# Kernel tuning notes

Measured on AMD Instinct MI355X. Metric: run time of the kernel, lower is better.

Reference implementation:

```python
import jax, jax.numpy as jnp
import numpy as np

GX, GY = 480, 360          # BEV grid (grid_size[0], grid_size[1])
C_OUT = 32                 # fea_compre
MAX_PT = 256               # max_pt_per_encode
NUM_VOX = GX * GY
BN_EPS = 1e-5


def setup_inputs() -> dict:
    key = jax.random.key(0)
    ks = jax.random.split(key, 12)
    B, N, F = 2, 100000, 7
    pt_fea = jax.random.normal(ks[0], (B, N, F), jnp.float32)
    xy_ind = jnp.stack([
        jax.random.randint(ks[1], (B, N), 0, GX),
        jax.random.randint(ks[2], (B, N), 0, GY),
    ], axis=-1).astype(jnp.int32)

    def lin(k, i, o):
        return 0.02 * jax.random.normal(k, (o, i), jnp.float32)

    inp = {"pt_fea": pt_fea, "xy_ind": xy_ind}
    dims = [(F, 64), (64, 128), (128, 256), (256, 512)]
    for j, (i, o) in enumerate(dims):
        inp[f"w{j}"] = lin(ks[3 + j], i, o)
        inp[f"b{j}"] = jnp.zeros((o,), jnp.float32)
    # BatchNorm (eval mode): bn0 on raw features, bn1..bn3 after linears 0..2
    for j, d in enumerate([F, 64, 128, 256]):
        inp[f"g{j}"] = jnp.ones((d,), jnp.float32)
        inp[f"be{j}"] = jnp.zeros((d,), jnp.float32)
        inp[f"m{j}"] = jnp.zeros((d,), jnp.float32)
        inp[f"v{j}"] = jnp.ones((d,), jnp.float32)
    inp["wc"] = lin(ks[7], 512, C_OUT)
    inp["bc"] = jnp.zeros((C_OUT,), jnp.float32)
    return inp


def _bn(x, g, b, m, v):
    return (x - m) * (g * jax.lax.rsqrt(v + BN_EPS)) + b


def reference(pt_fea, xy_ind,
              w0, b0, w1, b1, w2, b2, w3, b3,
              g0, be0, m0, v0, g1, be1, m1, v1,
              g2, be2, m2, v2, g3, be3, m3, v3,
              wc, bc):
    def pointnet(x):  # [N, 7] -> [N, 512]
        x = _bn(x, g0, be0, m0, v0)
        x = jax.nn.relu(_bn(x @ w0.T + b0, g1, be1, m1, v1))
        x = jax.nn.relu(_bn(x @ w1.T + b1, g2, be2, m2, v2))
        x = jax.nn.relu(_bn(x @ w2.T + b2, g3, be3, m3, v3))
        return x @ w3.T + b3

    def one_cloud(fea, xy):  # fea [N,7], xy [N,2] int
        N = fea.shape[0]
        vox = xy[:, 0] * GY + xy[:, 1]                      # linear voxel id
        # rank of each point within its voxel group (== grp_range_torch output)
        order = jnp.argsort(vox, stable=True)
        sid = vox[order]
        new_grp = jnp.concatenate([jnp.array([True]), sid[1:] != sid[:-1]])
        start = jax.lax.cummax(jnp.where(new_grp, jnp.arange(N), 0))
        rank_sorted = jnp.arange(N) - start
        rank = jnp.zeros((N,), rank_sorted.dtype).at[order].set(rank_sorted)
        remain = rank < MAX_PT                              # cap points per voxel

        pn = pointnet(fea)                                  # [N, 512]
        seg = jnp.where(remain, vox, NUM_VOX)               # dropped pts -> dummy seg
        maxf = jax.ops.segment_max(pn, seg, num_segments=NUM_VOX + 1)[:NUM_VOX]
        cnt = jax.ops.segment_sum(jnp.ones((N,), jnp.int32), seg,
                                  num_segments=NUM_VOX + 1)[:NUM_VOX]
        occ = (cnt > 0)[:, None]
        maxf = jnp.where(occ, maxf, 0.0)                    # kill -inf of empty voxels
        comp = jnp.where(occ, jax.nn.relu(maxf @ wc.T + bc), 0.0)  # [NUM_VOX, 32]
        return comp.reshape(GX, GY, C_OUT)

    grid = jax.vmap(one_cloud)(pt_fea, xy_ind)              # [B, GX, GY, 32]
    return jnp.transpose(grid, (0, 3, 1, 2))                # [B, 32, GX, GY]
```

## Files before the change

### kernel.cpp

```cpp
#include <hip/hip_runtime.h>

#define DEV __device__ __forceinline__

typedef _Float16 f16;
typedef __attribute__((ext_vector_type(8))) _Float16 half8;
typedef __attribute__((ext_vector_type(4))) _Float16 half4;
typedef __attribute__((ext_vector_type(4))) float floatx4;

constexpr int GXc = 480, GYc = 360;
constexpr int NVOX = GXc * GYc;
constexpr int BATCH = 2;
constexpr int NPT = 100000;
constexpr int FIN = 7;
constexpr int COUT = 32;
constexpr int MAXPT = 256;
constexpr float EPS = 1e-5f;
constexpr int NBLK = (NVOX + 255) / 256;
constexpr int FSTRIDE = NPT + 2;
constexpr int NB_PTS = (BATCH * NPT + 255) / 256;
constexpr int NB_FL  = (NPT + 255) / 256;
constexpr int ZB = 128;

DEV unsigned f2ord(float f) {
  unsigned b = __float_as_uint(f);
  return (b & 0x80000000u) ? ~b : (b | 0x80000000u);
}
DEV float ord2f(unsigned u) {
  return __uint_as_float((u & 0x80000000u) ? (u & 0x7FFFFFFFu) : ~u);
}

__global__ __launch_bounds__(256)
void k_foldcount(const float* __restrict__ w0, const float* __restrict__ b0,
                 const float* __restrict__ w1, const float* __restrict__ b1,
                 const float* __restrict__ w2, const float* __restrict__ b2,
                 const float* __restrict__ w3, const float* __restrict__ wc,
                 const float* __restrict__ g0, const float* __restrict__ be0, const float* __restrict__ m0, const float* __restrict__ v0,
                 const float* __restrict__ g1, const float* __restrict__ be1, const float* __restrict__ m1, const float* __restrict__ v1,
                 const float* __restrict__ g2, const float* __restrict__ be2, const float* __restrict__ m2, const float* __restrict__ v2,
                 const float* __restrict__ g3, const float* __restrict__ be3, const float* __restrict__ m3, const float* __restrict__ v3,
                 float* __restrict__ A0, float* __restrict__ c0,
                 f16* __restrict__ A1h, float* __restrict__ c1,
                 f16* __restrict__ A2h, float* __restrict__ c2,
                 f16* __restrict__ W3h, f16* __restrict__ Wch,
                 const int* __restrict__ xy, int* __restrict__ vox, int* __restrict__ cnt)
{
  int blk = blockIdx.x;
  if (blk < 512) {
    int id = blk * 256 + threadIdx.x;
    if (id < 131072) W3h[id] = (f16)w3[id];
    if (id < 32768) { int m = id >> 7; A2h[id] = (f16)(w2[id] * (g3[m] * rsqrtf(v3[m] + EPS))); }
    if (id < 16384) Wch[id] = (f16)wc[id];
    if (id < 8192)  { int m = id >> 6; A1h[id] = (f16)(w1[id] * (g2[m] * rsqrtf(v2[m] + EPS))); }
    if (id < 512) {
      int m = id >> 3, k = id & 7;
      A0[id] = (k < 7) ? w0[m * 7 + k] * (g0[k] * rsqrtf(v0[k] + EPS)) * (g1[m] * rsqrtf(v1[m] + EPS)) : 0.f;
    }
    if (id < 64) {
      float t1m = g1[id] * rsqrtf(v1[id] + EPS);
      float a = b0[id];
      for (int k = 0; k < 7; k++) {
        float t0k = g0[k] * rsqrtf(v0[k] + EPS);
        a += (be0[k] - m0[k] * t0k) * w0[id * 7 + k];
      }
      c0[id] = (a - m1[id]) * t1m + be1[id];
    }
    if (id < 128) c1[id] = (b1[id] - m2[id]) * (g2[id] * rsqrtf(v2[id] + EPS)) + be2[id];
    if (id < 256) c2[id] = (b2[id] - m3[id]) * (g3[id] * rsqrtf(v3[id] + EPS)) + be3[id];
  } else {
    int id = (blk - 512) * 256 + threadIdx.x;
    if (id >= BATCH * NPT) return;
    int b = id / NPT;
    int x = xy[id * 2 + 0], y = xy[id * 2 + 1];
    int v = x * GYc + y;
    vox[id] = v;
    atomicAdd(&cnt[b * NVOX + v], 1);
  }
}

__global__ __launch_bounds__(256)
void k_scan1(const int* __restrict__ cnt, int* __restrict__ slot, int* __restrict__ pofs,
             unsigned long long* __restrict__ bsum)
{
  __shared__ unsigned long long sc[256];
  int g = blockIdx.x, tid = threadIdx.x;
  int b = g / NBLK, blk = g % NBLK;
  int v = blk * 256 + tid;
  int c = (v < NVOX) ? cnt[b * NVOX + v] : 0;
  unsigned long long val = ((unsigned long long)(c > 0 ? 1u : 0u) << 32) | (unsigned)c;
  sc[tid] = val;
  __syncthreads();
  for (int off = 1; off < 256; off <<= 1) {
    unsigned long long t = (tid >= off) ? sc[tid - off] : 0ull;
    __syncthreads();
    sc[tid] += t;
    __syncthreads();
  }
  if (v < NVOX) {
    unsigned long long e = sc[tid] - val;
    slot[b * NVOX + v] = (int)(e >> 32);
    pofs[b * NVOX + v] = (int)(unsigned)e;
  }
  if (tid == 255) bsum[g] = sc[255];
}

__global__ __launch_bounds__(256)
void k_scan2(const unsigned long long* __restrict__ bsum, unsigned long long* __restrict__ boff,
             int* __restrict__ Stot)
{
  __shared__ unsigned long long sc[256];
  int b = blockIdx.x, tid = threadIdx.x;
  unsigned long long run = 0;
  for (int i0 = 0; i0 < NBLK; i0 += 256) {
    int i = i0 + tid;
    unsigned long long val = (i < NBLK) ? bsum[b * NBLK + i] : 0ull;
    sc[tid] = val;
    __syncthreads();
    for (int off = 1; off < 256; off <<= 1) {
      unsigned long long t = (tid >= off) ? sc[tid - off] : 0ull;
      __syncthreads();
      sc[tid] += t;
      __syncthreads();
    }
    if (i < NBLK) boff[b * NBLK + i] = run + sc[tid] - val;
    run += sc[255];
    __syncthreads();
  }
  if (tid == 0) Stot[b] = (int)(run >> 32);
}

__global__ __launch_bounds__(256)
void k_scan3(const int* __restrict__ cnt, int* __restrict__ slot, int* __restrict__ pofs,
             const unsigned long long* __restrict__ boff, int* __restrict__ occv,
             int* __restrict__ flag)
{
  int g = blockIdx.x, tid = threadIdx.x;
  int b = g / NBLK, blk = g % NBLK;
  int v = blk * 256 + tid;
  if (v >= NVOX) return;
  unsigned long long bo = boff[g];
  int s = slot[b * NVOX + v] + (int)(bo >> 32);
  int pp = pofs[b * NVOX + v] + (int)(unsigned)bo;
  slot[b * NVOX + v] = s;
  pofs[b * NVOX + v] = pp;
  int c = cnt[b * NVOX + v];
  if (c > 0) {
    occv[b * NPT + s] = v;
    int use = (c > MAXPT) ? MAXPT : c;
    bool capped = (c > MAXPT);
    bool span = ((pp >> 2) != ((pp + use - 1) >> 2));
    if (span || capped) atomicOr(&flag[b * FSTRIDE + s], 1);
    if (capped) atomicOr(&flag[b * FSTRIDE + s + 1], 1);
  }
}

__global__ __launch_bounds__(256)
void k_postscan(const int* __restrict__ vox, const int* __restrict__ pofs,
                const int* __restrict__ slot, int* __restrict__ tmp,
                int* __restrict__ order, int* __restrict__ sgrp,
                const int* __restrict__ flag, const int* __restrict__ Stot,
                int* __restrict__ nflag, int* __restrict__ flaglist)
{
  int blk = blockIdx.x;
  if (blk < NB_PTS) {
    int id = blk * 256 + threadIdx.x;
    if (id >= BATCH * NPT) return;
    int b = id / NPT, p = id - b * NPT;
    int v = vox[id];
    int r = atomicAdd(&tmp[b * NVOX + v], 1);
    int pos = pofs[b * NVOX + v] + r;
    order[b * NPT + pos] = p;
    sgrp[b * NPT + pos] = (r < MAXPT) ? slot[b * NVOX + v] : -2;
  } else {
    int rb = blk - NB_PTS;
    int b = rb / NB_FL;
    int s = (rb % NB_FL) * 256 + threadIdx.x;
    if (s >= Stot[b]) return;
    if (flag[b * FSTRIDE + s]) {
      int i = atomicAdd(&nflag[b], 1);
      flaglist[b * NPT + i] = s;
    }
  }
}

__global__ __launch_bounds__(256)
void k_mlp012(const float* __restrict__ X, const int* __restrict__ order,
              const float* __restrict__ A0, const float* __restrict__ c0,
              const f16* __restrict__ A1h, const float* __restrict__ c1,
              const f16* __restrict__ A2h, const float* __restrict__ c2,
              f16* __restrict__ H3, int P, int nmlp,
              unsigned* __restrict__ maxf, const int* __restrict__ flaglist,
              const int* __restrict__ nflag, int b, int scap)
{
  if (blockIdx.x >= nmlp) {
    int zb = blockIdx.x - nmlp;
    long long n = (long long)nflag[b] * 128;
    uint4 z; z.x = z.y = z.z = z.w = 0u;
    long long stride = (long long)ZB * 256;
    for (long long i = (long long)zb * 256 + threadIdx.x; i < n; i += stride) {
      int s = flaglist[b * NPT + (int)(i >> 7)];
      if (s < scap) ((uint4*)(maxf + (size_t)s * 512))[i & 127] = z;
    }
    return;
  }

  __shared__ __align__(16) char smem[65536];
  f16* H2s = (f16*)smem;
  f16* H1s = (f16*)(smem + 32768);
  f16* W1s = (f16*)(smem + 49152);
  float* A0s = (float*)smem;
  float* c0s = A0s + 512;
  f16* W2s = (f16*)(smem + 32768);

  const int tid = threadIdx.x;
  const int p0 = blockIdx.x * 128;
  const int wv = tid >> 6, ln = tid & 63;
  const int wp = (wv & 1) * 64, wm = (wv >> 1) * 64;
  const int l15 = ln & 15, lq = ln >> 4;

  A0s[tid] = A0[tid];
  A0s[tid + 256] = A0[tid + 256];
  if (tid < 64) c0s[tid] = c0[tid];
  #pragma unroll
  for (int it = 0; it < 4; it++) {
    int idx = it * 256 + tid;
    int r = idx >> 3, q = idx & 7;
    *(half8*)&W1s[r * 64 + (q ^ (r & 7)) * 8] = *(const half8*)(A1h + r * 64 + q * 8);
  }
  __syncthreads();

  {
    int p = tid >> 1, h = tid & 1;
    int pos = p0 + p; if (pos > P - 1) pos = P - 1;
    int pt = order[pos];
    float f[7];
    #pragma unroll
    for (int k = 0; k < 7; k++) f[k] = X[(size_t)pt * 7 + k];
    #pragma unroll
    for (int mm4 = 0; mm4 < 8; mm4++) {
      int mb = h * 32 + mm4 * 4;
      half4 ov;
      #pragma unroll
      for (int j = 0; j < 4; j++) {
        int m = mb + j;
        float a = c0s[m];
        #pragma unroll
        for (int k = 0; k < 7; k++) a += f[k] * A0s[m * 8 + k];
        ov[j] = (f16)(a > 0.f ? a : 0.f);
      }
      *(half4*)&H1s[p * 64 + ((mb >> 3) ^ (p & 7)) * 8 + (mb & 7)] = ov;
    }
  }
  __syncthreads();

  {
    floatx4 acc[4][4];
    #pragma unroll
    for (int i = 0; i < 4; i++)
      #pragma unroll
      for (int j = 0; j < 4; j++) acc[i][j] = (floatx4)0.f;
    #pragma unroll
    for (int k0 = 0; k0 < 64; k0 += 32) {
      half8 af[4], bf[4];
      #pragma unroll
      for (int i = 0; i < 4; i++) {
        int row = wp + i * 16 + l15;
        af[i] = *(const half8*)&H1s[row * 64 + (((k0 >> 3) + lq) ^ (row & 7)) * 8];
      }
      #pragma unroll
      for (int j = 0; j < 4; j++) {
        int row = wm + j * 16 + l15;
        bf[j] = *(const half8*)&W1s[row * 64 + (((k0 >> 3) + lq) ^ (row & 7)) * 8];
      }
      #pragma unroll
      for (int i = 0; i < 4; i++)
        #pragma unroll
        for (int j = 0; j < 4; j++)
          acc[i][j] = __builtin_amdgcn_mfma_f32_16x16x32_f16(af[i], bf[j], acc[i][j], 0, 0, 0);
    }
    float c1j[4];
    #pragma unroll
    for (int j = 0; j < 4; j++) c1j[j] = c1[wm + j * 16 + l15];
    #pragma unroll
    for (int i = 0; i < 4; i++) {
      #pragma unroll
      for (int r = 0; r < 4; r++) {
        int row = wp + i * 16 + lq * 4 + r;
        #pragma unroll
        for (int j = 0; j < 4; j++) {
          int col = wm + j * 16 + l15;
          float v = acc[i][j][r] + c1j[j];
          if (v < 0.f) v = 0.f;
          H2s[row * 128 + ((col >> 3) ^ (row & 7)) * 8 + (col & 7)] = (f16)v;
        }
      }
    }
  }
  __syncthreads();

  for (int mc = 0; mc < 2; mc++) {
    floatx4 acc[4][4];
    #pragma unroll
    for (int i = 0; i < 4; i++)
      #pragma unroll
      for (int j = 0; j < 4; j++) acc[i][j] = (floatx4)0.f;
    for (int k0 = 0; k0 < 128; k0 += 32) {
      __syncthreads();
      #pragma unroll
      for (int it = 0; it < 2; it++) {
        int idx = it * 256 + tid;
        int r = idx >> 2, q = idx & 3;
        *(half8*)&W2s[r * 40 + q * 8] =
            *(const half8*)(A2h + (size_t)(mc * 128 + r) * 128 + k0 + q * 8);
      }
      __syncthreads();
      half8 af[4], bf[4];
      #pragma unroll
      for (int i = 0; i < 4; i++) {
        int row = wp + i * 16 + l15;
        af[i] = *(const half8*)&H2s[row * 128 + (((k0 >> 3) + lq) ^ (row & 7)) * 8];
      }
      #pragma unroll
      for (int j = 0; j < 4; j++)
        bf[j] = *(const half8*)&W2s[(wm + j * 16 + l15) * 40 + lq * 8];
      #pragma unroll
      for (int i = 0; i < 4; i++)
        #pragma unroll
        for (int j = 0; j < 4; j++)
          acc[i][j] = __builtin_amdgcn_mfma_f32_16x16x32_f16(af[i], bf[j], acc[i][j], 0, 0, 0);
    }
    float c2j[4];
    #pragma unroll
    for (int j = 0; j < 4; j++) c2j[j] = c2[mc * 128 + wm + j * 16 + l15];
    #pragma unroll
    for (int i = 0; i < 4; i++) {
      #pragma unroll
      for (int r = 0; r < 4; r++) {
        int prow = p0 + wp + i * 16 + lq * 4 + r;
        if (prow < P) {
          #pragma unroll
          for (int j = 0; j < 4; j++) {
            int col = mc * 128 + wm + j * 16 + l15;
            float v = acc[i][j][r] + c2j[j];
            if (v < 0.f) v = 0.f;
            H3[(size_t)prow * 256 + col] = (f16)v;
          }
        }
      }
    }
  }
}

constexpr int LW = 40;

__global__ __launch_bounds__(256)
void k_gemm16_smax(const f16* __restrict__ A, const f16* __restrict__ W,
                   const float* __restrict__ bias, int P,
                   unsigned* __restrict__ maxf, const int* __restrict__ sg,
                   int chunk0, int rest, int scap, int nxpad)
{
  constexpr int K = 256, M = 512;
  __shared__ f16 Xs[128 * LW];
  __shared__ f16 Ws[128 * LW];
  const int tid = threadIdx.x;
  const int xb = blockIdx.x % nxpad;
  const int yb = blockIdx.x / nxpad;
  if (xb * 128 >= P) return;
  const int p0 = xb * 128;
  const int m0 = yb * 128;
  const int wv = tid >> 6, ln = tid & 63;
  const int wp = (wv & 1) * 64, wm = (wv >> 1) * 64;
  const int l15 = ln & 15, lq = ln >> 4;

  floatx4 acc[4][4];
  #pragma unroll
  for (int i = 0; i < 4; i++)
    #pragma unroll
    for (int j = 0; j < 4; j++) acc[i][j] = (floatx4)0.f;

  const int sr = tid >> 2, sq = tid & 3;
  int pr = p0 + sr;      if (pr > P - 1) pr = P - 1;
  int pr2 = p0 + sr + 64; if (pr2 > P - 1) pr2 = P - 1;
  const f16* aptr0 = A + (size_t)pr * K + sq * 8;
  const f16* aptr1 = A + (size_t)pr2 * K + sq * 8;
  const f16* wptr0 = W + (size_t)(m0 + sr) * K + sq * 8;
  const f16* wptr1 = W + (size_t)(m0 + sr + 64) * K + sq * 8;

  half8 ra0 = *(const half8*)(aptr0);
  half8 ra1 = *(const half8*)(aptr1);
  half8 rw0 = *(const half8*)(wptr0);
  half8 rw1 = *(const half8*)(wptr1);

  #pragma unroll
  for (int k0 = 0; k0 < K; k0 += 32) {
    *(half8*)&Xs[sr * LW + sq * 8]        = ra0;
    *(half8*)&Xs[(sr + 64) * LW + sq * 8] = ra1;
    *(half8*)&Ws[sr * LW + sq * 8]        = rw0;
    *(half8*)&Ws[(sr + 64) * LW + sq * 8] = rw1;
    if (k0 + 32 < K) {
      ra0 = *(const half8*)(aptr0 + k0 + 32);
      ra1 = *(const half8*)(aptr1 + k0 + 32);
      rw0 = *(const half8*)(wptr0 + k0 + 32);
      rw1 = *(const half8*)(wptr1 + k0 + 32);
    }
    __syncthreads();
    half8 af[4], bf[4];
    #pragma unroll
    for (int i = 0; i < 4; i++)
      af[i] = *(const half8*)&Xs[(wp + i * 16 + l15) * LW + lq * 8];
    #pragma unroll
    for (int j = 0; j < 4; j++)
      bf[j] = *(const half8*)&Ws[(wm + j * 16 + l15) * LW + lq * 8];
    #pragma unroll
    for (int i = 0; i < 4; i++)
      #pragma unroll
      for (int j = 0; j < 4; j++)
        acc[i][j] = __builtin_amdgcn_mfma_f32_16x16x32_f16(af[i], bf[j], acc[i][j], 0, 0, 0);
    __syncthreads();
  }

  float bj[4];
  #pragma unroll
  for (int j = 0; j < 4; j++) bj[j] = bias[m0 + wm + j * 16 + l15];
  const int cbase = m0 + wm + l15;

  #pragma unroll
  for (int i = 0; i < 4; i++) {
    int pr0 = p0 + wp + i * 16 + lq * 4;
    float run[4];
    int gcur = -1;
    bool openL = false;

    auto flushrun = [&](int gc, bool open) {
      if (gc >= scap) return;
      unsigned* row = maxf + (size_t)gc * M + cbase;
      if (open) {
        #pragma unroll
        for (int j = 0; j < 4; j++) atomicMax(row + j * 16, f2ord(run[j]));
      } else {
        #pragma unroll
        for (int j = 0; j < 4; j++) row[j * 16] = f2ord(run[j]);
      }
    };

    int glast = (chunk0 + pr0 > 0) ? sg[pr0 - 1] : -1;
    #pragma unroll
    for (int r = 0; r < 4; r++) {
      int pos = pr0 + r;
      int g = (pos < P) ? sg[pos] : -1;
      if (g >= 0) {
        if (g == gcur) {
          #pragma unroll
          for (int j = 0; j < 4; j++) run[j] = fmaxf(run[j], acc[i][j][r] + bj[j]);
        } else {
          if (gcur >= 0) flushrun(gcur, openL);
          gcur = g;
          openL = (glast == g) || (glast == -2);
          #pragma unroll
          for (int j = 0; j < 4; j++) run[j] = acc[i][j][r] + bj[j];
        }
      } else {
        if (gcur >= 0) { flushrun(gcur, openL || (g == -2)); gcur = -1; }
      }
      glast = g;
    }
    if (gcur >= 0) {
      int gnext = (pr0 + 4 < rest) ? sg[pr0 + 4] : -1;
      flushrun(gcur, openL || (gnext == gcur) || (gnext == -2));
    }
  }
}

__global__ __launch_bounds__(256)
void k_compress_mfma(const unsigned* __restrict__ maxf, const f16* __restrict__ Wch,
                     const float* __restrict__ bc, const int* __restrict__ Stot,
                     float* __restrict__ outc, int scap)
{
  int S = Stot[0]; if (S > scap) S = scap;
  const int s0 = blockIdx.x * 128;
  if (s0 >= S) return;
  __shared__ f16 Wcs[32 * 512];
  __shared__ f16 Xs[128 * LW];
  const int tid = threadIdx.x;
  const int wv = tid >> 6, ln = tid & 63;
  const int l15 = ln & 15, lq = ln >> 4;

  #pragma unroll
  for (int it = 0; it < 8; it++) {
    int idx = it * 256 + tid;
    int row = idx >> 6, oct = idx & 63;
    *(half8*)&Wcs[row * 512 + (oct >> 3) * 64 + ((oct & 7) ^ (row & 7)) * 8] =
        *(const half8*)(Wch + (size_t)row * 512 + oct * 8);
  }

  const unsigned* aq[4];
  #pragma unroll
  for (int l = 0; l < 4; l++) {
    int idx = l * 256 + tid;
    int r = idx >> 3, q = idx & 7;
    int srow = s0 + r; if (srow > S - 1) srow = S - 1;
    aq[l] = maxf + (size_t)srow * 512 + q * 4;
  }

  floatx4 acc[2][2];
  #pragma unroll
  for (int i = 0; i < 2; i++)
    #pragma unroll
    for (int j = 0; j < 2; j++) acc[i][j] = (floatx4)0.f;

  uint4 pf[4];
  #pragma unroll
  for (int l = 0; l < 4; l++) pf[l] = *(const uint4*)(aq[l]);

  #pragma unroll
  for (int k0 = 0; k0 < 512; k0 += 32) {
    #pragma unroll
    for (int l = 0; l < 4; l++) {
      int idx = l * 256 + tid;
      int r = idx >> 3, q = idx & 7;
      half4 hv;
      hv[0] = (f16)ord2f(pf[l].x); hv[1] = (f16)ord2f(pf[l].y);
      hv[2] = (f16)ord2f(pf[l].z); hv[3] = (f16)ord2f(pf[l].w);
      *(half4*)&Xs[r * LW + q * 4] = hv;
    }
    if (k0 + 32 < 512) {
      #pragma unroll
      for (int l = 0; l < 4; l++) pf[l] = *(const uint4*)(aq[l] + k0 + 32);
    }
    __syncthreads();
    half8 af[2], bf[2];
    #pragma unroll
    for (int i = 0; i < 2; i++)
      af[i] = *(const half8*)&Xs[(wv * 32 + i * 16 + l15) * LW + lq * 8];
    int oct = (k0 >> 3) + lq;
    int hi64 = (oct >> 3) * 64, lo = oct & 7;
    #pragma unroll
    for (int j = 0; j < 2; j++) {
      int row = j * 16 + l15;
      bf[j] = *(const half8*)&Wcs[row * 512 + hi64 + (lo ^ (row & 7)) * 8];
    }
    #pragma unroll
    for (int i = 0; i < 2; i++)
      #pragma unroll
      for (int j = 0; j < 2; j++)
        acc[i][j] = __builtin_amdgcn_mfma_f32_16x16x32_f16(af[i], bf[j], acc[i][j], 0, 0, 0);
    __syncthreads();
  }

  #pragma unroll
  for (int i = 0; i < 2; i++) {
    int sb = s0 + wv * 32 + i * 16 + lq * 4;
    #pragma unroll
    for (int r = 0; r < 4; r++) {
      int s = sb + r;
      if (s < S) {
        #pragma unroll
        for (int j = 0; j < 2; j++) {
          int c = j * 16 + l15;
          float v = acc[i][j][r] + bc[c];
          outc[(size_t)s * COUT + c] = v > 0.f ? v : 0.f;
        }
      }
    }
  }
}

__global__ __launch_bounds__(256)
void k_scatter_out(const float* __restrict__ outc, const int* __restrict__ cnt,
                   const int* __restrict__ slot, float* __restrict__ outb, int scap)
{
  int v = blockIdx.x * 256 + threadIdx.x;
  if (v >= NVOX) return;
  bool occ = cnt[v] > 0;
  int s = slot[v];
  float4 a[8];
  if (occ && s < scap) {
    #pragma unroll
    for (int q = 0; q < 8; q++) a[q] = *(const float4*)(outc + (size_t)s * COUT + q * 4);
  } else {
    #pragma unroll
    for (int q = 0; q < 8; q++) { a[q].x = 0.f; a[q].y = 0.f; a[q].z = 0.f; a[q].w = 0.f; }
  }
  const float* af = (const float*)a;
  #pragma unroll
  for (int c = 0; c < 32; c++) outb[(size_t)c * NVOX + v] = af[c];
}

extern "C" void kernel_launch(void* const* d_in, const int* in_sizes, int n_in,
                              void* d_out, int out_size, void* d_ws, size_t ws_size,
                              hipStream_t stream) {
  (void)in_sizes; (void)n_in; (void)out_size;
  const float* pt_fea = (const float*)d_in[0];
  const int*   xy     = (const int*)d_in[1];
  const float* w0 = (const float*)d_in[2];  const float* b0 = (const float*)d_in[3];
  const float* w1 = (const float*)d_in[4];  const float* b1 = (const float*)d_in[5];
  const float* w2 = (const float*)d_in[6];  const float* b2 = (const float*)d_in[7];
  const float* w3 = (const float*)d_in[8];  const float* b3 = (const float*)d_in[9];
  const float* g0 = (const float*)d_in[10]; const float* be0 = (const float*)d_in[11];
  const float* m0 = (const float*)d_in[12]; const float* v0  = (const float*)d_in[13];
  const float* g1 = (const float*)d_in[14]; const float* be1 = (const float*)d_in[15];
  const float* m1 = (const float*)d_in[16]; const float* v1  = (const float*)d_in[17];
  const float* g2 = (const float*)d_in[18]; const float* be2 = (const float*)d_in[19];
  const float* m2 = (const float*)d_in[20]; const float* v2  = (const float*)d_in[21];
  const float* g3 = (const float*)d_in[22]; const float* be3 = (const float*)d_in[23];
  const float* m3 = (const float*)d_in[24]; const float* v3  = (const float*)d_in[25];
  const float* wc = (const float*)d_in[26]; const float* bc = (const float*)d_in[27];
  float* outp = (float*)d_out;

  char* base = (char*)d_ws;
  size_t off = 0;
  auto alloc = [&](size_t n) -> void* {
    void* p = base + off;
    off = (off + n + 255) & ~(size_t)255;
    return p;
  };
  float* A0f = (float*)alloc(512 * 4);    float* c0f = (float*)alloc(64 * 4);
  f16* A1h = (f16*)alloc(8192 * 2);       float* c1f = (float*)alloc(128 * 4);
  f16* A2h = (f16*)alloc(32768 * 2);      float* c2f = (float*)alloc(256 * 4);
  f16* W3h = (f16*)alloc(131072 * 2);
  f16* Wch = (f16*)alloc(16384 * 2);
  int* vox  = (int*)alloc((size_t)BATCH * NPT * 4);
  int* slot = (int*)alloc((size_t)BATCH * NVOX * 4);
  int* pofs = (int*)alloc((size_t)BATCH * NVOX * 4);
  unsigned long long* bsum = (unsigned long long*)alloc((size_t)BATCH * NBLK * 8);
  unsigned long long* boff = (unsigned long long*)alloc((size_t)BATCH * NBLK * 8);
  int* Stot = (int*)alloc((size_t)BATCH * 4);
  int* occv = (int*)alloc((size_t)BATCH * NPT * 4);
  int* order = (int*)alloc((size_t)BATCH * NPT * 4);
  int* sgrp  = (int*)alloc((size_t)BATCH * NPT * 4);
  int* flist = (int*)alloc((size_t)BATCH * NPT * 4);
  float* outc = (float*)alloc((size_t)NPT * COUT * 4);
  size_t zoff0 = off;
  int* cnt  = (int*)alloc((size_t)BATCH * NVOX * 4);
  int* tmp  = (int*)alloc((size_t)BATCH * NVOX * 4);
  int* flag = (int*)alloc((size_t)BATCH * FSTRIDE * 4);
  int* nflag = (int*)alloc((size_t)BATCH * 4);
  size_t zlen = off - zoff0;

  int scap = NPT;
  size_t remain = (ws_size > off) ? ws_size - off : 0;
  size_t minH = (size_t)128 * 256 * 2;
  if (remain < (size_t)scap * 512 * 4 + minH) {
    size_t avail = (remain > minH) ? remain - minH : 0;
    scap = (int)(avail / 2048);
    if (scap < 1) scap = 1;
  }
  unsigned* maxf = (unsigned*)alloc((size_t)scap * 512 * 4);

  size_t hrem = (ws_size > off) ? ws_size - off : 0;
  int P = (int)((hrem / ((size_t)256 * 2)) & ~(size_t)127);
  if (P > NPT) P = ((NPT + 127) / 128) * 128;
  if (P < 128) P = 128;
  f16* H3 = (f16*)alloc((size_t)P * 256 * 2);

  hipMemsetAsync(base + zoff0, 0, zlen, stream);

  k_foldcount<<<512 + NB_PTS, 256, 0, stream>>>(w0, b0, w1, b1, w2, b2, w3, wc,
                                                g0, be0, m0, v0, g1, be1, m1, v1,
                                                g2, be2, m2, v2, g3, be3, m3, v3,
                                                A0f, c0f, A1h, c1f, A2h, c2f, W3h, Wch,
                                                xy, vox, cnt);
  k_scan1<<<BATCH * NBLK, 256, 0, stream>>>(cnt, slot, pofs, bsum);
  k_scan2<<<BATCH, 256, 0, stream>>>(bsum, boff, Stot);
  k_scan3<<<BATCH * NBLK, 256, 0, stream>>>(cnt, slot, pofs, boff, occv, flag);
  k_postscan<<<NB_PTS + BATCH * NB_FL, 256, 0, stream>>>(vox, pofs, slot, tmp, order, sgrp,
                                                         flag, Stot, nflag, flist);

  for (int b = 0; b < BATCH; b++) {
    for (int p0 = 0; p0 < NPT; p0 += P) {
      int pc = (NPT - p0 < P) ? (NPT - p0) : P;
      int nmlp = (pc + 127) / 128;
      int gext = (p0 == 0) ? ZB : 0;
      k_mlp012<<<nmlp + gext, 256, 0, stream>>>(pt_fea + (size_t)b * NPT * FIN,
                                                order + (size_t)b * NPT + p0,
                                                A0f, c0f, A1h, c1f, A2h, c2f,
                                                H3, pc, nmlp,
                                                maxf, flist, nflag, b, scap);
      int nxpad = (nmlp + 7) & ~7;
      k_gemm16_smax<<<nxpad * 4, 256, 0, stream>>>(H3, W3h, b3, pc,
                                                   maxf, sgrp + (size_t)b * NPT + p0,
                                                   p0, NPT - p0, scap, nxpad);
    }
    k_compress_mfma<<<(NPT + 127) / 128, 256, 0, stream>>>(maxf, Wch, bc, Stot + b,
                                                           outc, scap);
    k_scatter_out<<<(NVOX + 255) / 256, 256, 0, stream>>>(outc, cnt + (size_t)b * NVOX,
                                                          slot + (size_t)b * NVOX,
                                                          outp + (size_t)b * COUT * NVOX,
                                                          scap);
  }
}
```

Before: 529.8 us.

## Restructure MLP layer-2 weight staging, loop gemm over output slices, shrink compress tiles

In k_mlp012, each 128-row half of the layer-2 weights is now staged into swizzled shared memory once, instead of in four k-steps with two barriers each, which removes six barriers per half. k_gemm16_smax now has each block loop over all four 128-column output slices rather than using a 2D grid. This cuts blocks by 4x but serialises work per block and reloads the A rows from global four times. k_compress_mfma moves to 64-row tiles with one MFMA row-tile per wave, giving more blocks at lower per-wave work.

```diff
diff --git a/kernel.cpp b/kernel.cpp
--- a/kernel.cpp
+++ b/kernel.cpp
@@ -209,7 +209,7 @@
   f16* W1s = (f16*)(smem + 49152);
   float* A0s = (float*)smem;
   float* c0s = A0s + 512;
-  f16* W2s = (f16*)(smem + 32768);
+  f16* W2f = (f16*)(smem + 32768);
 
   const int tid = threadIdx.x;
   const int p0 = blockIdx.x * 128;
@@ -295,24 +295,25 @@
       }
     }
   }
-  __syncthreads();
 
   for (int mc = 0; mc < 2; mc++) {
+    __syncthreads();
+    #pragma unroll
+    for (int it = 0; it < 8; it++) {
+      int idx = it * 256 + tid;
+      int row = idx >> 4, oct = idx & 15;
+      *(half8*)&W2f[row * 128 + (oct >> 3) * 64 + ((oct & 7) ^ (row & 7)) * 8] =
+          *(const half8*)(A2h + (size_t)(mc * 128 + row) * 128 + oct * 8);
+    }
+    __syncthreads();
+
     floatx4 acc[4][4];
     #pragma unroll
     for (int i = 0; i < 4; i++)
       #pragma unroll
       for (int j = 0; j < 4; j++) acc[i][j] = (floatx4)0.f;
+    #pragma unroll
     for (int k0 = 0; k0 < 128; k0 += 32) {
-      __syncthreads();
-      #pragma unroll
-      for (int it = 0; it < 2; it++) {
-        int idx = it * 256 + tid;
-        int r = idx >> 2, q = idx & 3;
-        *(half8*)&W2s[r * 40 + q * 8] =
-            *(const half8*)(A2h + (size_t)(mc * 128 + r) * 128 + k0 + q * 8);
-      }
-      __syncthreads();
       half8 af[4], bf[4];
       #pragma unroll
       for (int i = 0; i < 4; i++) {
@@ -320,8 +321,11 @@
         af[i] = *(const half8*)&H2s[row * 128 + (((k0 >> 3) + lq) ^ (row & 7)) * 8];
       }
       #pragma unroll
-      for (int j = 0; j < 4; j++)
-        bf[j] = *(const half8*)&W2s[(wm + j * 16 + l15) * 40 + lq * 8];
+      for (int j = 0; j < 4; j++) {
+        int row = wm + j * 16 + l15;
+        int oct = (k0 >> 3) + lq;
+        bf[j] = *(const half8*)&W2f[row * 128 + (oct >> 3) * 64 + ((oct & 7) ^ (row & 7)) * 8];
+      }
       #pragma unroll
       for (int i = 0; i < 4; i++)
         #pragma unroll
@@ -356,116 +360,116 @@
 void k_gemm16_smax(const f16* __restrict__ A, const f16* __restrict__ W,
                    const float* __restrict__ bias, int P,
                    unsigned* __restrict__ maxf, const int* __restrict__ sg,
-                   int chunk0, int rest, int scap, int nxpad)
+                   int chunk0, int rest, int scap)
 {
   constexpr int K = 256, M = 512;
   __shared__ f16 Xs[128 * LW];
   __shared__ f16 Ws[128 * LW];
   const int tid = threadIdx.x;
-  const int xb = blockIdx.x % nxpad;
-  const int yb = blockIdx.x / nxpad;
-  if (xb * 128 >= P) return;
-  const int p0 = xb * 128;
-  const int m0 = yb * 128;
+  const int p0 = blockIdx.x * 128;
   const int wv = tid >> 6, ln = tid & 63;
   const int wp = (wv & 1) * 64, wm = (wv >> 1) * 64;
   const int l15 = ln & 15, lq = ln >> 4;
 
-  floatx4 acc[4][4];
-  #pragma unroll
-  for (int i = 0; i < 4; i++)
-    #pragma unroll
-    for (int j = 0; j < 4; j++) acc[i][j] = (floatx4)0.f;
-
   const int sr = tid >> 2, sq = tid & 3;
-  int pr = p0 + sr;      if (pr > P - 1) pr = P - 1;
+  int pr = p0 + sr;       if (pr > P - 1) pr = P - 1;
   int pr2 = p0 + sr + 64; if (pr2 > P - 1) pr2 = P - 1;
   const f16* aptr0 = A + (size_t)pr * K + sq * 8;
   const f16* aptr1 = A + (size_t)pr2 * K + sq * 8;
-  const f16* wptr0 = W + (size_t)(m0 + sr) * K + sq * 8;
-  const f16* wptr1 = W + (size_t)(m0 + sr + 64) * K + sq * 8;
-
-  half8 ra0 = *(const half8*)(aptr0);
-  half8 ra1 = *(const half8*)(aptr1);
-  half8 rw0 = *(const half8*)(wptr0);
-  half8 rw1 = *(const half8*)(wptr1);
-
-  #pragma unroll
-  for (int k0 = 0; k0 < K; k0 += 32) {
-    *(half8*)&Xs[sr * LW + sq * 8]        = ra0;
-    *(half8*)&Xs[(sr + 64) * LW + sq * 8] = ra1;
-    *(half8*)&Ws[sr * LW + sq * 8]        = rw0;
-    *(half8*)&Ws[(sr + 64) * LW + sq * 8] = rw1;
-    if (k0 + 32 < K) {
-      ra0 = *(const half8*)(aptr0 + k0 + 32);
-      ra1 = *(const half8*)(aptr1 + k0 + 32);
-      rw0 = *(const half8*)(wptr0 + k0 + 32);
-      rw1 = *(const half8*)(wptr1 + k0 + 32);
-    }
-    __syncthreads();
-    half8 af[4], bf[4];
+
+  for (int ms = 0; ms < 4; ms++) {
+    const int m0 = ms * 128;
+    const f16* wptr0 = W + (size_t)(m0 + sr) * K + sq * 8;
+    const f16* wptr1 = W + (size_t)(m0 + sr + 64) * K + sq * 8;
+
+    floatx4 acc[4][4];
     #pragma unroll
     for (int i = 0; i < 4; i++)
-      af[i] = *(const half8*)&Xs[(wp + i * 16 + l15) * LW + lq * 8];
-    #pragma unroll
-    for (int j = 0; j < 4; j++)
-      bf[j] = *(const half8*)&Ws[(wm + j * 16 + l15) * LW + lq * 8];
-    #pragma unroll
-    for (int i = 0; i < 4; i++)
+      #pragma unroll
+      for (int j = 0; j < 4; j++) acc[i][j] = (floatx4)0.f;
+
+    half8 ra0 = *(const half8*)(aptr0);
+    half8 ra1 = *(const half8*)(aptr1);
+    half8 rw0 = *(const half8*)(wptr0);
+    half8 rw1 = *(const half8*)(wptr1);
+
+    #pragma unroll
+    for (int k0 = 0; k0 < K; k0 += 32) {
+      *(half8*)&Xs[sr * LW + sq * 8]        = ra0;
+      *(half8*)&Xs[(sr + 64) * LW + sq * 8] = ra1;
+      *(half8*)&Ws[sr * LW + sq * 8]        = rw0;
+      *(half8*)&Ws[(sr + 64) * LW + sq * 8] = rw1;
+      if (k0 + 32 < K) {
+        ra0 = *(const half8*)(aptr0 + k0 + 32);
+        ra1 = *(const half8*)(aptr1 + k0 + 32);
+        rw0 = *(const half8*)(wptr0 + k0 + 32);
+        rw1 = *(const half8*)(wptr1 + k0 + 32);
+      }
+      __syncthreads();
+      half8 af[4], bf[4];
+      #pragma unroll
+      for (int i = 0; i < 4; i++)
+        af[i] = *(const half8*)&Xs[(wp + i * 16 + l15) * LW + lq * 8];
       #pragma unroll
       for (int j = 0; j < 4; j++)
-        acc[i][j] = __builtin_amdgcn_mfma_f32_16x16x32_f16(af[i], bf[j], acc[i][j], 0, 0, 0);
-    __syncthreads();
-  }
-
-  float bj[4];
-  #pragma unroll
-  for (int j = 0; j < 4; j++) bj[j] = bias[m0 + wm + j * 16 + l15];
-  const int cbase = m0 + wm + l15;
-
-  #pragma unroll
-  for (int i = 0; i < 4; i++) {
-    int pr0 = p0 + wp + i * 16 + lq * 4;
-    float run[4];
-    int gcur = -1;
-    bool openL = false;
-
-    auto flushrun = [&](int gc, bool open) {
-      if (gc >= scap) return;
-      unsigned* row = maxf + (size_t)gc * M + cbase;
-      if (open) {
+        bf[j] = *(const half8*)&Ws[(wm + j * 16 + l15) * LW + lq * 8];
+      #pragma unroll
+      for (int i = 0; i < 4; i++)
         #pragma unroll
-        for (int j = 0; j < 4; j++) atomicMax(row + j * 16, f2ord(run[j]));
-      } else {
-        #pragma unroll
-        for (int j = 0; j < 4; j++) row[j * 16] = f2ord(run[j]);
-      }
-    };
-
-    int glast = (chunk0 + pr0 > 0) ? sg[pr0 - 1] : -1;
-    #pragma unroll
-    for (int r = 0; r < 4; r++) {
-      int pos = pr0 + r;
-      int g = (pos < P) ? sg[pos] : -1;
-      if (g >= 0) {
-        if (g == gcur) {
+        for (int j = 0; j < 4; j++)
+          acc[i][j] = __builtin_amdgcn_mfma_f32_16x16x32_f16(af[i], bf[j], acc[i][j], 0, 0, 0);
+      __syncthreads();
+    }
+
+    float bj[4];
+    #pragma unroll
+    for (int j = 0; j < 4; j++) bj[j] = bias[m0 + wm + j * 16 + l15];
+    const int cbase = m0 + wm + l15;
+
+    #pragma unroll
+    for (int i = 0; i < 4; i++) {
+      int pr0 = p0 + wp + i * 16 + lq * 4;
+      float run[4];
+      int gcur = -1;
+      bool openL = false;
+
+      auto flushrun = [&](int gc, bool open) {
+        if (gc >= scap) return;
+        unsigned* row = maxf + (size_t)gc * M + cbase;
+        if (open) {
           #pragma unroll
-          for (int j = 0; j < 4; j++) run[j] = fmaxf(run[j], acc[i][j][r] + bj[j]);
+          for (int j = 0; j < 4; j++) atomicMax(row + j * 16, f2ord(run[j]));
         } else {
-          if (gcur >= 0) flushrun(gcur, openL);
-          gcur = g;
-          openL = (glast == g) || (glast == -2);
           #pragma unroll
-          for (int j = 0; j < 4; j++) run[j] = acc[i][j][r] + bj[j];
+          for (int j = 0; j < 4; j++) row[j * 16] = f2ord(run[j]);
         }
-      } else {
-        if (gcur >= 0) { flushrun(gcur, openL || (g == -2)); gcur = -1; }
-      }
-      glast = g;
-    }
-    if (gcur >= 0) {
-      int gnext = (pr0 + 4 < rest) ? sg[pr0 + 4] : -1;
-      flushrun(gcur, openL || (gnext == gcur) || (gnext == -2));
+      };
+
+      int glast = (chunk0 + pr0 > 0) ? sg[pr0 - 1] : -1;
+      #pragma unroll
+      for (int r = 0; r < 4; r++) {
+        int pos = pr0 + r;
+        int g = (pos < P) ? sg[pos] : -1;
+        if (g >= 0) {
+          if (g == gcur) {
+            #pragma unroll
+            for (int j = 0; j < 4; j++) run[j] = fmaxf(run[j], acc[i][j][r] + bj[j]);
+          } else {
+            if (gcur >= 0) flushrun(gcur, openL);
+            gcur = g;
+            openL = (glast == g) || (glast == -2);
+            #pragma unroll
+            for (int j = 0; j < 4; j++) run[j] = acc[i][j][r] + bj[j];
+          }
+        } else {
+          if (gcur >= 0) { flushrun(gcur, openL || (g == -2)); gcur = -1; }
+        }
+        glast = g;
+      }
+      if (gcur >= 0) {
+        int gnext = (pr0 + 4 < rest) ? sg[pr0 + 4] : -1;
+        flushrun(gcur, openL || (gnext == gcur) || (gnext == -2));
+      }
     }
   }
 }
@@ -476,10 +480,10 @@
                      float* __restrict__ outc, int scap)
 {
   int S = Stot[0]; if (S > scap) S = scap;
-  const int s0 = blockIdx.x * 128;
+  const int s0 = blockIdx.x * 64;
   if (s0 >= S) return;
   __shared__ f16 Wcs[32 * 512];
-  __shared__ f16 Xs[128 * LW];
+  __shared__ f16 Xs[64 * LW];
   const int tid = threadIdx.x;
   const int wv = tid >> 6, ln = tid & 63;
   const int l15 = ln & 15, lq = ln >> 4;
@@ -492,29 +496,26 @@
         *(const half8*)(Wch + (size_t)row * 512 + oct * 8);
   }
 
-  const unsigned* aq[4];
+  const unsigned* aq[2];
   #pragma unroll
-  for (int l = 0; l < 4; l++) {
+  for (int l = 0; l < 2; l++) {
     int idx = l * 256 + tid;
     int r = idx >> 3, q = idx & 7;
     int srow = s0 + r; if (srow > S - 1) srow = S - 1;
     aq[l] = maxf + (size_t)srow * 512 + q * 4;
   }
 
-  floatx4 acc[2][2];
-  #pragma unroll
-  for (int i = 0; i < 2; i++)
-    #pragma unroll
-    for (int j = 0; j < 2; j++) acc[i][j] = (floatx4)0.f;
-
-  uint4 pf[4];
-  #pragma unroll
-  for (int l = 0; l < 4; l++) pf[l] = *(const uint4*)(aq[l]);
+  floatx4 acc[2];
+  acc[0] = (floatx4)0.f; acc[1] = (floatx4)0.f;
+
+  uint4 pf[2];
+  pf[0] = *(const uint4*)(aq[0]);
+  pf[1] = *(const uint4*)(aq[1]);
 
   #pragma unroll
   for (int k0 = 0; k0 < 512; k0 += 32) {
     #pragma unroll
-    for (int l = 0; l < 4; l++) {
+    for (int l = 0; l < 2; l++) {
       int idx = l * 256 + tid;
       int r = idx >> 3, q = idx & 7;
       half4 hv;
@@ -523,14 +524,12 @@
       *(half4*)&Xs[r * LW + q * 4] = hv;
     }
     if (k0 + 32 < 512) {
-      #pragma unroll
-      for (int l = 0; l < 4; l++) pf[l] = *(const uint4*)(aq[l] + k0 + 32);
-    }
-    __syncthreads();
-    half8 af[2], bf[2];
-    #pragma unroll
-    for (int i = 0; i < 2; i++)
-      af[i] = *(const half8*)&Xs[(wv * 32 + i * 16 + l15) * LW + lq * 8];
+      pf[0] = *(const uint4*)(aq[0] + k0 + 32);
+      pf[1] = *(const uint4*)(aq[1] + k0 + 32);
+    }
+    __syncthreads();
+    half8 af, bf[2];
+    af = *(const half8*)&Xs[(wv * 16 + l15) * LW + lq * 8];
     int oct = (k0 >> 3) + lq;
     int hi64 = (oct >> 3) * 64, lo = oct & 7;
     #pragma unroll
@@ -539,16 +538,13 @@
       bf[j] = *(const half8*)&Wcs[row * 512 + hi64 + (lo ^ (row & 7)) * 8];
     }
     #pragma unroll
-    for (int i = 0; i < 2; i++)
-      #pragma unroll
-      for (int j = 0; j < 2; j++)
-        acc[i][j] = __builtin_amdgcn_mfma_f32_16x16x32_f16(af[i], bf[j], acc[i][j], 0, 0, 0);
-    __syncthreads();
-  }
-
-  #pragma unroll
-  for (int i = 0; i < 2; i++) {
-    int sb = s0 + wv * 32 + i * 16 + lq * 4;
+    for (int j = 0; j < 2; j++)
+      acc[j] = __builtin_amdgcn_mfma_f32_16x16x32_f16(af, bf[j], acc[j], 0, 0, 0);
+    __syncthreads();
+  }
+
+  {
+    int sb = s0 + wv * 16 + lq * 4;
     #pragma unroll
     for (int r = 0; r < 4; r++) {
       int s = sb + r;
@@ -556,7 +552,7 @@
         #pragma unroll
         for (int j = 0; j < 2; j++) {
           int c = j * 16 + l15;
-          float v = acc[i][j][r] + bc[c];
+          float v = acc[j][r] + bc[c];
           outc[(size_t)s * COUT + c] = v > 0.f ? v : 0.f;
         }
       }
@@ -675,13 +671,12 @@
                                                 A0f, c0f, A1h, c1f, A2h, c2f,
                                                 H3, pc, nmlp,
                                                 maxf, flist, nflag, b, scap);
-      int nxpad = (nmlp + 7) & ~7;
-      k_gemm16_smax<<<nxpad * 4, 256, 0, stream>>>(H3, W3h, b3, pc,
-                                                   maxf, sgrp + (size_t)b * NPT + p0,
-                                                   p0, NPT - p0, scap, nxpad);
-    }
-    k_compress_mfma<<<(NPT + 127) / 128, 256, 0, stream>>>(maxf, Wch, bc, Stot + b,
-                                                           outc, scap);
+      k_gemm16_smax<<<nmlp, 256, 0, stream>>>(H3, W3h, b3, pc,
+                                              maxf, sgrp + (size_t)b * NPT + p0,
+                                              p0, NPT - p0, scap);
+    }
+    k_compress_mfma<<<(NPT + 63) / 64, 256, 0, stream>>>(maxf, Wch, bc, Stot + b,
+                                                         outc, scap);
     k_scatter_out<<<(NVOX + 255) / 256, 256, 0, stream>>>(outc, cnt + (size_t)b * NVOX,
                                                           slot + (size_t)b * NVOX,
                                                           outp + (size_t)b * COUT * NVOX,
```

Result: slower. 636.4 us (+20.1%).
